# Performance work log

Hardware: AMD Instinct MI355X
Metric: run time of the kernel (lower is better)

## Reference

```python
import jax, jax.numpy as jnp
import numpy as np

B, NN, DEG = 64, 256, 8
N = B * NN
E = N * DEG
IN_N, IN_E = 128, 16
TOOL, PROC = 16, 12
TP = TOOL * PROC
H1 = 384

def _lin(key, i, o, s=0.05):
    k1, k2 = jax.random.split(key)
    return (jax.random.normal(k1, (i, o), jnp.float32) * s,
            jax.random.normal(k2, (o,), jnp.float32) * s)

def setup_inputs():
    ks = jax.random.split(jax.random.key(0), 40)
    inp = {}
    inp["ns"] = jax.random.normal(ks[0], (N, IN_N), jnp.float32)
    inp["es"] = jax.random.normal(ks[1], (E, IN_E), jnp.float32)
    inp["dm"] = jax.random.normal(ks[2], (N, NN), jnp.float32)
    inp["mask_fv"] = (jax.random.uniform(ks[3], (N, TP)) > 0.3).astype(jnp.float32)
    dst = jnp.repeat(jnp.arange(N, dtype=jnp.int32), DEG)  # fixed in-degree DEG
    src = (dst // NN) * NN + jax.random.randint(ks[4], (E,), 0, NN, dtype=jnp.int32)
    inp["src"], inp["dst"] = src, dst
    sizes = [(IN_N, H1), (H1 + 32, H1), (H1, TP)]
    for i, (cin, cout) in enumerate(sizes, 1):
        inp[f"Wm{i}"], inp[f"bm{i}"] = _lin(ks[5 + 3 * i], 2 * cin + IN_E, cin)
        inp[f"Wu{i}"], inp[f"bu{i}"] = _lin(ks[6 + 3 * i], 5 * cin, cout)
        inp[f"bng{i}"] = jnp.ones((cout,), jnp.float32)
        inp[f"bnb{i}"] = jnp.zeros((cout,), jnp.float32)
        inp[f"Wx{i}"], inp[f"bx{i}"] = _lin(ks[7 + 3 * i], cout, cout)
    inp["W1"], inp["b1"] = _lin(ks[20], NN, 64)
    inp["W2"], inp["b2"] = _lin(ks[21], 64, 32)
    inp["W3"], inp["b3"] = _lin(ks[22], NN, 64)
    inp["W4"], inp["b4"] = _lin(ks[23], 64, NN)
    return inp

def pna_conv(src, dst, h, e, Wm, bm, Wu, bu, bng, bnb, Wx, bx, relu_out):
    # DGL PNAConvTower: msg = M(cat(h_src, h_dst, e)); aggregate mean/max/sum/std per dst node;
    # U(cat(h, aggs)); BatchNorm (training stats); mixing Linear + LeakyReLU(0.01).
    cin = h.shape[1]
    msg = h[src] @ Wm[:cin] + h[dst] @ Wm[cin:2 * cin] + e @ Wm[2 * cin:] + bm  # [E, cin]
    cnt = jax.ops.segment_sum(jnp.ones((msg.shape[0],), msg.dtype), dst, N)[:, None]
    s = jax.ops.segment_sum(msg, dst, N)
    mean = s / cnt
    mx = jax.ops.segment_max(msg, dst, N)
    msq = jax.ops.segment_sum(msg * msg, dst, N) / cnt
    std = jnp.sqrt(jax.nn.relu(msq - mean * mean) + 1e-30)
    u = jnp.concatenate([h, mean, mx, s, std], axis=-1) @ Wu + bu  # [N, cout]
    u = (u - u.mean(0)) / jnp.sqrt(u.var(0) + 1e-5) * bng + bnb  # BatchNorm1d, training mode
    out = jax.nn.leaky_relu(u @ Wx + bx, 0.01)  # mixing layer
    return jax.nn.relu(out) if relu_out else out

def reference(ns, es, dm, mask_fv, Wm1, bm1, Wu1, bu1, bng1, bnb1, Wx1, bx1, Wm2, bm2, Wu2, bu2, bng2, bnb2, Wx2, bx2, Wm3, bm3, Wu3, bu3, bng3, bnb3, Wx3, bx3, W1, b1, W2, b2, W3, b3, W4, b4, src, dst):
    d2 = (dm @ W1 + b1) @ W2 + b2  # [N, 32]
    h1 = pna_conv(src, dst, ns, es, Wm1, bm1, Wu1, bu1, bng1, bnb1, Wx1, bx1, True)
    h2 = pna_conv(src, dst, jnp.concatenate([h1, d2], -1), es, Wm2, bm2, Wu2, bu2, bng2, bnb2, Wx2, bx2, True)
    h3 = pna_conv(src, dst, h2, es, Wm3, bm3, Wu3, bu3, bng3, bnb3, Wx3, bx3, False)  # [N, TP]
    nm = h3.max(-1).reshape(B, NN)
    g = jax.nn.sigmoid(jax.nn.relu(nm @ W3 + b3) @ W4 + b4)  # [B, NN]
    feat = (g.reshape(N, 1) * h3).reshape(B, -1)  # [B, NN*TP]
    feat = jnp.where(mask_fv.reshape(B, -1) == 0, -1e5, feat)
    return jax.nn.softmax(feat, -1)
```

## Files before the change

### kernel.cpp

```cpp
#include <hip/hip_runtime.h>
#include <hip/hip_bf16.h>

#define NNODE 16384

typedef short v8s __attribute__((ext_vector_type(8)));
typedef float v4f __attribute__((ext_vector_type(4)));
typedef unsigned short us16;

__device__ __forceinline__ us16 f2bf(float v) {
    unsigned u = __float_as_uint(v);
    unsigned r = (u + 0x7FFF + ((u >> 16) & 1)) >> 16;
    return (us16)r;
}
__device__ __forceinline__ float bf2f(us16 s) {
    return __uint_as_float(((unsigned)s) << 16);
}

template<int EPI, int OUT, int ACC, int BM, int NB>
__global__ __launch_bounds__(256, 3)
void mgemm6(const us16* __restrict__ Ah, const us16* __restrict__ Al,
            int ldA, int K,
            const us16* __restrict__ Bh, const us16* __restrict__ Bl, int KC,
            const float* __restrict__ CfIn, int ldCin,
            float* __restrict__ Cf, us16* __restrict__ Ch, us16* __restrict__ Cl,
            int ldC, int Ncol, const float* __restrict__ bias)
{
    constexpr int MF = BM / 32;
    __shared__ __align__(16) us16 AhS[BM * 64];
    __shared__ __align__(16) us16 AlS[BM * 64];
    const int bm = blockIdx.x * BM;
    const int bn0 = blockIdx.y * (64 * NB);
    const int tid = threadIdx.x;
    const int lane = tid & 63, wid = tid >> 6;
    const int wm = wid >> 1, wn = wid & 1;
    const int r16 = lane & 15, q = lane >> 4;
    v4f acc[NB][MF][2];
#pragma unroll
    for (int b = 0; b < NB; b++)
#pragma unroll
        for (int i = 0; i < MF; i++)
#pragma unroll
            for (int j = 0; j < 2; j++) acc[b][i][j] = (v4f){0.f, 0.f, 0.f, 0.f};

    const int srow = tid >> 3;
    const int sc8  = tid & 7;
    const int cbw  = (bn0 >> 4) + wn * 2;
    const int nK = (K + 63) >> 6;
    for (int s = 0; s < nK; s++) {
        const int k0 = s << 6;
#pragma unroll
        for (int p = 0; p < BM / 32; p++) {
            int row = p * 32 + srow;
            int gk = k0 + sc8 * 8;
            v8s hv = (v8s){0,0,0,0,0,0,0,0};
            v8s lv = (v8s){0,0,0,0,0,0,0,0};
            if (gk < K) {
                size_t go = (size_t)(bm + row) * ldA + gk;
                hv = *(const v8s*)(const void*)(Ah + go);
                lv = *(const v8s*)(const void*)(Al + go);
            }
            int bo = row * 128 + ((sc8 * 16) ^ ((row & 7) << 4));
            *(v8s*)(void*)((char*)AhS + bo) = hv;
            *(v8s*)(void*)((char*)AlS + bo) = lv;
        }
        __syncthreads();
#pragma unroll
        for (int kc = 0; kc < 2; kc++) {
            int kchunk = (k0 >> 5) + kc;
            v8s bfh[NB][2], bfl[NB][2];
#pragma unroll
            for (int nb = 0; nb < NB; nb++)
#pragma unroll
                for (int nf = 0; nf < 2; nf++) {
                    int colblk = cbw + nb * 4 + nf;
                    size_t fo = ((size_t)(colblk * KC + kchunk) * 64 + lane) * 8;
                    bfh[nb][nf] = *(const v8s*)(const void*)(Bh + fo);
                    bfl[nb][nf] = *(const v8s*)(const void*)(Bl + fo);
                }
#pragma unroll
            for (int mf = 0; mf < MF; mf++) {
                int arow = wm * (BM / 2) + mf * 16 + r16;
                int ao = arow * 128 + (((kc * 64) + q * 16) ^ ((arow & 7) << 4));
                v8s ah = *(const v8s*)(const void*)((const char*)AhS + ao);
                v8s al = *(const v8s*)(const void*)((const char*)AlS + ao);
#pragma unroll
                for (int nb = 0; nb < NB; nb++)
#pragma unroll
                    for (int nf = 0; nf < 2; nf++) {
                        acc[nb][mf][nf] = __builtin_amdgcn_mfma_f32_16x16x32_bf16(ah, bfh[nb][nf], acc[nb][mf][nf], 0, 0, 0);
                        acc[nb][mf][nf] = __builtin_amdgcn_mfma_f32_16x16x32_bf16(al, bfh[nb][nf], acc[nb][mf][nf], 0, 0, 0);
                        acc[nb][mf][nf] = __builtin_amdgcn_mfma_f32_16x16x32_bf16(ah, bfl[nb][nf], acc[nb][mf][nf], 0, 0, 0);
                    }
            }
        }
        __syncthreads();
    }
#pragma unroll
    for (int nb = 0; nb < NB; nb++)
#pragma unroll
        for (int mf = 0; mf < MF; mf++)
#pragma unroll
            for (int nf = 0; nf < 2; nf++) {
                int col = bn0 + nb * 64 + wn * 32 + nf * 16 + r16;
                if (col < Ncol) {
                    float bv = bias ? bias[col] : 0.f;
#pragma unroll
                    for (int r = 0; r < 4; r++) {
                        int row = bm + wm * (BM / 2) + mf * 16 + q * 4 + r;
                        float v = acc[nb][mf][nf][r] + bv;
                        if (ACC) v += CfIn[(size_t)row * ldCin + col];
                        if (EPI == 1) v = fmaxf(v, 0.f);
                        if (EPI == 2) v = (v > 0.f) ? v : 0.01f * v;
                        size_t o = (size_t)row * ldC + col;
                        if (OUT == 0) {
                            Cf[o] = v;
                        } else {
                            us16 h = f2bf(v);
                            Ch[o] = h;
                            Cl[o] = f2bf(v - bf2f(h));
                        }
                    }
                }
            }
}

struct FrD {
    const float* W;
    us16* Bh;
    us16* Bl;
    int ldW, Kv, Nv, Na, KC, mode, cin, blk0;
};
struct FrPack { FrD d[16]; int nd; };

__global__ __launch_bounds__(256) void prep_fr_all(FrPack p)
{
    int b = blockIdx.x;
    int i = 0;
    for (int j = 1; j < p.nd; j++) if (b >= p.d[j].blk0) i = j;
    const FrD dd = p.d[i];
    int idx = (b - dd.blk0) * 256 + threadIdx.x;
    if (idx >= dd.Na * dd.KC * 32) return;
    int e = idx & 7, lane = (idx >> 3) & 63, rem = idx >> 9;
    int kchunk = rem % dd.KC, colblk = rem / dd.KC;
    int n = colblk * 16 + (lane & 15);
    int k = kchunk * 32 + (lane >> 4) * 8 + e;
    float v = 0.f;
    if (dd.mode == 0) {
        if (k < dd.Kv && n < dd.Nv) v = dd.W[(size_t)k * dd.ldW + n];
    } else if (dd.mode == 1) {
        int cin = dd.cin, cout = dd.Nv;
        if (n < cout && k < 3 * cin) {
            if (k < cin)          v = dd.W[(size_t)(cin + k) * cout + n] * 0.125f + dd.W[(size_t)(3 * cin + k) * cout + n];
            else if (k < 2 * cin) v = dd.W[(size_t)(2 * cin + (k - cin)) * cout + n];
            else                  v = dd.W[(size_t)(4 * cin + (k - 2 * cin)) * cout + n];
        }
    }
    us16 h = f2bf(v);
    dd.Bh[idx] = h;
    dd.Bl[idx] = f2bf(v - bf2f(h));
}

__global__ void prep_fr_wx(const float* __restrict__ Wx, const float* __restrict__ scale,
                           us16* __restrict__ Bh, us16* __restrict__ Bl,
                           int K, int N, int KC)
{
    int idx = blockIdx.x * 256 + threadIdx.x;
    if (idx >= N * KC * 32) return;
    int e = idx & 7, lane = (idx >> 3) & 63, rem = idx >> 9;
    int kchunk = rem % KC, colblk = rem / KC;
    int n = colblk * 16 + (lane & 15);
    int k = kchunk * 32 + (lane >> 4) * 8 + e;
    float v = (k < K && n < N) ? Wx[(size_t)k * N + n] * scale[k] : 0.f;
    us16 h = f2bf(v);
    Bh[idx] = h;
    Bl[idx] = f2bf(v - bf2f(h));
}

__global__ void w12frag_k(const float* __restrict__ W1, const float* __restrict__ W2,
                          us16* __restrict__ Bh, us16* __restrict__ Bl)
{
    int idx = blockIdx.x * 256 + threadIdx.x;
    if (idx >= 64 * 8 * 32) return;
    int e = idx & 7, lane = (idx >> 3) & 63, rem = idx >> 9;
    int kchunk = rem % 8, colblk = rem / 8;
    int n = colblk * 16 + (lane & 15);
    int k = kchunk * 32 + (lane >> 4) * 8 + e;
    float v = 0.f;
    if (n < 32 && k < 256) {
        for (int j = 0; j < 64; j++) v = fmaf(W1[(size_t)k * 64 + j], W2[(size_t)j * 32 + n], v);
    }
    us16 h = f2bf(v);
    Bh[idx] = h;
    Bl[idx] = f2bf(v - bf2f(h));
}

__global__ void bias12_k(const float* __restrict__ b1, const float* __restrict__ W2,
                         const float* __restrict__ b2, float* __restrict__ b12)
{
    int n = threadIdx.x;
    if (n >= 32) return;
    float s = b2[n];
    for (int j = 0; j < 64; j++) s = fmaf(b1[j], W2[(size_t)j * 32 + n], s);
    b12[n] = s;
}

__global__ __launch_bounds__(256) void bias2p_k(const float* __restrict__ Wx,
    const float* __restrict__ bx, const float* __restrict__ shift,
    float* __restrict__ bias2, int K, int N)
{
    int n = blockIdx.x, tid = threadIdx.x;
    float s = 0.f;
    for (int k = tid; k < K; k += 256) s = fmaf(shift[k], Wx[(size_t)k * N + n], s);
    __shared__ float red[256];
    red[tid] = s; __syncthreads();
    for (int st = 128; st > 0; st >>= 1) { if (tid < st) red[tid] += red[tid + st]; __syncthreads(); }
    if (tid == 0) bias2[n] = red[0] + bx[n];
}

__global__ void prep_biasMU(const float* __restrict__ bm, const float* __restrict__ bu,
                            float* __restrict__ o, int cin, int cout)
{
    int i = blockIdx.x * 256 + threadIdx.x;
    if (i >= 2 * cin + cout) return;
    float v;
    if (i < cin)          v = 0.f;
    else if (i < 2 * cin) v = bm[i - cin];
    else                  v = bu[i - 2 * cin];
    o[i] = v;
}

__global__ void csplit2_k(const float* __restrict__ ns, us16* __restrict__ Xh, us16* __restrict__ Xl,
                          const float* __restrict__ dm, us16* __restrict__ Dh, us16* __restrict__ Dl)
{
    int b = blockIdx.x;
    if (b < 8192) {
        int idx = b * 256 + threadIdx.x;
        int rrow = idx >> 7, c = idx & 127;
        float v = ns[idx];
        us16 h = f2bf(v);
        size_t o = (size_t)rrow * 512 + c;
        Xh[o] = h;
        Xl[o] = f2bf(v - bf2f(h));
    } else {
        int idx = (b - 8192) * 256 + threadIdx.x;
        float v = dm[idx];
        us16 h = f2bf(v);
        Dh[idx] = h;
        Dl[idx] = f2bf(v - bf2f(h));
    }
}

__global__ void csplit_k(const float* __restrict__ src, int ldS, int w,
                         us16* __restrict__ Xh, us16* __restrict__ Xl,
                         int ldX, int offX)
{
    int idx = blockIdx.x * 256 + threadIdx.x;
    if (idx >= NNODE * w) return;
    int rrow = idx / w, c = idx - rrow * w;
    float v = src[(size_t)rrow * ldS + c];
    us16 h = f2bf(v);
    size_t o = (size_t)rrow * ldX + offX + c;
    Xh[o] = h;
    Xl[o] = f2bf(v - bf2f(h));
}

__global__ __launch_bounds__(256)
void agg2_k(const float* __restrict__ H2, const float* __restrict__ es,
            const int* __restrict__ src, const float* __restrict__ Wme,
            us16* __restrict__ Xh, us16* __restrict__ Xl,
            int cin, int ldH, int ldX, int offX)
{
    const int g = blockIdx.x;
    const int c0 = blockIdx.y * 64;
    const int qz = blockIdx.z;
    const int tid = threadIdx.x;
    const int nl = tid >> 6, c = tid & 63;
    const int cc = c0 + c;
    const bool act = cc < cin;
    __shared__ float esl[4][128];
    __shared__ int srcl[512];
    {
        int e0 = g * 2048 + qz * 512;
        for (int i = tid; i < 512; i += 256) srcl[i] = src[e0 + i] - g * 256;
    }
    float wreg[16];
#pragma unroll
    for (int j = 0; j < 16; j++) wreg[j] = act ? Wme[j * cin + cc] : 0.f;
    __syncthreads();
    const float* Hsrc = H2 + (size_t)(g * 256) * ldH + c0;
    const float* Hdst = H2 + (size_t)(g * 256) * ldH + cin + c0;
    for (int i = 0; i < 16; i++) {
        const int vl = qz * 64 + i * 4 + nl;
        {
            const float* ep = es + (size_t)(g * 256 + vl) * 128;
            esl[nl][c] = ep[c];
            esl[nl][64 + c] = ep[64 + c];
        }
        __syncthreads();
        if (act) {
            float hd = Hdst[(size_t)vl * ldH + c];
            float sum = 0.f, sq = 0.f, mx = -INFINITY;
#pragma unroll
            for (int e = 0; e < 8; e++) {
                int sl = srcl[(i * 4 + nl) * 8 + e];
                float m = hd + Hsrc[(size_t)sl * ldH + c];
                float4 e0 = *(const float4*)&esl[nl][e * 16 + 0];
                float4 e1 = *(const float4*)&esl[nl][e * 16 + 4];
                float4 e2 = *(const float4*)&esl[nl][e * 16 + 8];
                float4 e3 = *(const float4*)&esl[nl][e * 16 + 12];
                m = fmaf(e0.x, wreg[0], m);  m = fmaf(e0.y, wreg[1], m);
                m = fmaf(e0.z, wreg[2], m);  m = fmaf(e0.w, wreg[3], m);
                m = fmaf(e1.x, wreg[4], m);  m = fmaf(e1.y, wreg[5], m);
                m = fmaf(e1.z, wreg[6], m);  m = fmaf(e1.w, wreg[7], m);
                m = fmaf(e2.x, wreg[8], m);  m = fmaf(e2.y, wreg[9], m);
                m = fmaf(e2.z, wreg[10], m); m = fmaf(e2.w, wreg[11], m);
                m = fmaf(e3.x, wreg[12], m); m = fmaf(e3.y, wreg[13], m);
                m = fmaf(e3.z, wreg[14], m); m = fmaf(e3.w, wreg[15], m);
                sum += m;
                sq = fmaf(m, m, sq);
                mx = fmaxf(mx, m);
            }
            float mean = sum * 0.125f, msq = sq * 0.125f;
            float stdv = sqrtf(fmaxf(msq - mean * mean, 0.f) + 1e-30f);
            size_t o = (size_t)(g * 256 + vl) * ldX + offX + cc;
            us16 h;
            h = f2bf(sum);  Xh[o] = h;            Xl[o] = f2bf(sum - bf2f(h));
            h = f2bf(mx);   Xh[o + cin] = h;      Xl[o + cin] = f2bf(mx - bf2f(h));
            h = f2bf(stdv); Xh[o + 2 * cin] = h;  Xl[o + 2 * cin] = f2bf(stdv - bf2f(h));
        }
        __syncthreads();
    }
}

__global__ void bnstats1s_k(const us16* __restrict__ uh, const us16* __restrict__ ul,
                            float* __restrict__ part, int cout)
{
    int c = threadIdx.x;
    if (c >= cout) return;
    int r0 = blockIdx.x * 64;
    float s = 0.f, q = 0.f;
    for (int r = r0; r < r0 + 64; r++) {
        size_t o = (size_t)r * cout + c;
        float v = bf2f(uh[o]) + bf2f(ul[o]);
        s += v;
        q = fmaf(v, v, q);
    }
    part[(size_t)blockIdx.x * cout + c] = s;
    part[(size_t)(256 + blockIdx.x) * cout + c] = q;
}

__global__ void bnstats2_k(const float* __restrict__ part, const float* __restrict__ bng,
                           const float* __restrict__ bnb, float* __restrict__ scale,
                           float* __restrict__ shift, int cout)
{
    int c = threadIdx.x;
    if (c >= cout) return;
    float s = 0.f, q = 0.f;
    for (int b = 0; b < 256; b++) { s += part[(size_t)b * cout + c]; q += part[(size_t)(256 + b) * cout + c]; }
    float mean = s / 16384.f;
    float var  = q / 16384.f - mean * mean;
    float sc   = bng[c] / sqrtf(var + 1e-5f);
    scale[c] = sc;
    shift[c] = bnb[c] - mean * sc;
}

__global__ void rowmax_k(const float* __restrict__ h3, float* __restrict__ nm)
{
    int wave = threadIdx.x >> 6;
    int lane = threadIdx.x & 63;
    int node = blockIdx.x * 4 + wave;
    const float* row = h3 + (size_t)node * 192;
    float m = -INFINITY;
    for (int t = lane; t < 192; t += 64) m = fmaxf(m, row[t]);
#pragma unroll
    for (int off = 32; off > 0; off >>= 1) m = fmaxf(m, __shfl_down(m, off, 64));
    if (lane == 0) nm[node] = m;
}

__global__ __launch_bounds__(256) void g_k(const float* __restrict__ nm,
    const float* __restrict__ W3, const float* __restrict__ b3,
    const float* __restrict__ W4, const float* __restrict__ b4,
    float* __restrict__ g)
{
    __shared__ float row[256];
    __shared__ float t1[64];
    int b = blockIdx.x, tid = threadIdx.x;
    row[tid] = nm[b * 256 + tid];
    __syncthreads();
    if (tid < 64) {
        float a = b3[tid];
        for (int k = 0; k < 256; k++) a = fmaf(row[k], W3[k * 64 + tid], a);
        t1[tid] = fmaxf(a, 0.f);
    }
    __syncthreads();
    float a = b4[tid];
    for (int j = 0; j < 64; j++) a = fmaf(t1[j], W4[j * 256 + tid], a);
    g[b * 256 + tid] = 1.f / (1.f + expf(-a));
}

__global__ __launch_bounds__(256) void sm1_k(const float* __restrict__ mask,
    const float* __restrict__ g, const float* __restrict__ h3, float* __restrict__ part)
{
    int b = blockIdx.x, s = blockIdx.y, tid = threadIdx.x;
    float l[24];
#pragma unroll
    for (int t = 0; t < 24; t++) {
        int i = s * 6144 + t * 256 + tid;
        size_t idx = (size_t)b * 49152 + i;
        float mk = mask[idx];
        l[t] = (mk == 0.f) ? -1e5f : g[b * 256 + i / 192] * h3[idx];
    }
    float m = -INFINITY;
#pragma unroll
    for (int t = 0; t < 24; t++) m = fmaxf(m, l[t]);
    __shared__ float red[256];
    red[tid] = m; __syncthreads();
    for (int st = 128; st > 0; st >>= 1) { if (tid < st) red[tid] = fmaxf(red[tid], red[tid + st]); __syncthreads(); }
    m = red[0]; __syncthreads();
    float z = 0.f;
#pragma unroll
    for (int t = 0; t < 24; t++) z += expf(l[t] - m);
    red[tid] = z; __syncthreads();
    for (int st = 128; st > 0; st >>= 1) { if (tid < st) red[tid] += red[tid + st]; __syncthreads(); }
    if (tid == 0) { part[(b * 8 + s) * 2] = m; part[(b * 8 + s) * 2 + 1] = red[0]; }
}

__global__ void sm2_k(const float* __restrict__ part, float* __restrict__ mz)
{
    int b = threadIdx.x;
    if (b >= 64) return;
    float M = -INFINITY;
    for (int s = 0; s < 8; s++) M = fmaxf(M, part[(b * 8 + s) * 2]);
    float Z = 0.f;
    for (int s = 0; s < 8; s++) Z += part[(b * 8 + s) * 2 + 1] * expf(part[(b * 8 + s) * 2] - M);
    mz[b * 2] = M;
    mz[b * 2 + 1] = 1.f / Z;
}

__global__ __launch_bounds__(256) void sm3_k(const float* __restrict__ mask,
    const float* __restrict__ g, const float* __restrict__ h3,
    const float* __restrict__ mz, float* __restrict__ out)
{
    int b = blockIdx.x, s = blockIdx.y, tid = threadIdx.x;
    float M = mz[b * 2], invZ = mz[b * 2 + 1];
#pragma unroll
    for (int t = 0; t < 24; t++) {
        int i = s * 6144 + t * 256 + tid;
        size_t idx = (size_t)b * 49152 + i;
        float mk = mask[idx];
        float v = (mk == 0.f) ? -1e5f : g[b * 256 + i / 192] * h3[idx];
        out[idx] = expf(v - M) * invZ;
    }
}

extern "C" void kernel_launch(void* const* d_in, const int* in_sizes, int n_in,
                              void* d_out, int out_size, void* d_ws, size_t ws_size,
                              hipStream_t stream)
{
    const float* ns   = (const float*)d_in[0];
    const float* es   = (const float*)d_in[1];
    const float* dm   = (const float*)d_in[2];
    const float* mask = (const float*)d_in[3];
    const int*   src  = (const int*)d_in[4];
    const float* Wm1 = (const float*)d_in[6],  *bm1 = (const float*)d_in[7];
    const float* Wu1 = (const float*)d_in[8],  *bu1 = (const float*)d_in[9];
    const float* bng1= (const float*)d_in[10], *bnb1= (const float*)d_in[11];
    const float* Wx1 = (const float*)d_in[12], *bx1 = (const float*)d_in[13];
    const float* Wm2 = (const float*)d_in[14], *bm2 = (const float*)d_in[15];
    const float* Wu2 = (const float*)d_in[16], *bu2 = (const float*)d_in[17];
    const float* bng2= (const float*)d_in[18], *bnb2= (const float*)d_in[19];
    const float* Wx2 = (const float*)d_in[20], *bx2 = (const float*)d_in[21];
    const float* Wm3 = (const float*)d_in[22], *bm3 = (const float*)d_in[23];
    const float* Wu3 = (const float*)d_in[24], *bu3 = (const float*)d_in[25];
    const float* bng3= (const float*)d_in[26], *bnb3= (const float*)d_in[27];
    const float* Wx3 = (const float*)d_in[28], *bx3 = (const float*)d_in[29];
    const float* W1 = (const float*)d_in[30], *b1 = (const float*)d_in[31];
    const float* W2 = (const float*)d_in[32], *b2 = (const float*)d_in[33];
    const float* W3 = (const float*)d_in[34], *b3 = (const float*)d_in[35];
    const float* W4 = (const float*)d_in[36], *b4 = (const float*)d_in[37];
    float* out = (float*)d_out;

    const int N = NNODE;
    char* base = (char*)d_ws;
    size_t off = 0;
    auto alloc = [&](size_t bytes) -> void* {
        void* p = base + off;
        off = (off + bytes + 255) & ~(size_t)255;
        return p;
    };
    us16* Xh = (us16*)alloc((size_t)N * 1728 * 2);
    us16* Xl = (us16*)alloc((size_t)N * 1728 * 2);
    float* H2   = (float*)alloc((size_t)N * 1216 * 4);
    us16* uh = (us16*)alloc((size_t)N * 384 * 2);
    us16* ul = (us16*)alloc((size_t)N * 384 * 2);
    us16* dmh = (us16*)alloc((size_t)N * 256 * 2);
    us16* dml = (us16*)alloc((size_t)N * 256 * 2);
    float* h3b  = (float*)alloc((size_t)N * 192 * 4);
    float* d2f  = (float*)alloc((size_t)N * 32 * 4);
    float* part = (float*)alloc((size_t)512 * 384 * 4);
    float* scale= (float*)alloc(384 * 4);
    float* shift= (float*)alloc(384 * 4);
    float* bias2= (float*)alloc(384 * 4);
    float* b12  = (float*)alloc(32 * 4);
    float* biasMU1 = (float*)alloc(640 * 4);
    float* biasMU2 = (float*)alloc(1216 * 4);
    float* biasMU3 = (float*)alloc(960 * 4);
    float* nm   = (float*)alloc((size_t)N * 4);
    float* gbuf = (float*)alloc((size_t)N * 4);
    float* smp  = (float*)alloc(64 * 8 * 2 * 4);
    float* smz  = (float*)alloc(64 * 2 * 4);
    auto aw = [&](size_t elems) -> us16* { return (us16*)alloc(elems * 2); };
    us16 *BM1h = aw((size_t)640 * 4 * 32),    *BM1l = aw((size_t)640 * 4 * 32);
    us16 *BA1h = aw((size_t)384 * 12 * 32),   *BA1l = aw((size_t)384 * 12 * 32);
    us16 *BX1h = aw((size_t)384 * 12 * 32),   *BX1l = aw((size_t)384 * 12 * 32);
    us16 *BM2h = aw((size_t)1280 * 14 * 32),  *BM2l = aw((size_t)1280 * 14 * 32);
    us16 *BA2h = aw((size_t)384 * 40 * 32),   *BA2l = aw((size_t)384 * 40 * 32);
    us16 *BX2h = aw((size_t)384 * 12 * 32),   *BX2l = aw((size_t)384 * 12 * 32);
    us16 *BM3h = aw((size_t)1024 * 12 * 32),  *BM3l = aw((size_t)1024 * 12 * 32);
    us16 *BA3h = aw((size_t)192 * 36 * 32),   *BA3l = aw((size_t)192 * 36 * 32);
    us16 *BX3h = aw((size_t)192 * 6 * 32),    *BX3l = aw((size_t)192 * 6 * 32);
    us16 *B12h = aw((size_t)64 * 8 * 32),     *B12l = aw((size_t)64 * 8 * 32);

    auto gp = [](size_t n) { return dim3((unsigned)((n + 255) / 256)); };
    auto fsec = [](us16* b, int c0, int KC) { return b + (size_t)(c0 / 16) * KC * 512; };

    FrPack pk;
    int nd = 0, blk = 0;
    auto addD = [&](const float* W, us16* Bh, us16* Bl, int ldW, int Kv, int Nv, int Na, int KC, int mode, int cin) {
        pk.d[nd] = {W, Bh, Bl, ldW, Kv, Nv, Na, KC, mode, cin, blk};
        blk += (Na * KC * 32 + 255) / 256;
        nd++;
    };
    addD(Wm1,             fsec(BM1h,0,4),    fsec(BM1l,0,4),    128, 128, 128, 128, 4, 0, 0);
    addD(Wm1 + 128*128,   fsec(BM1h,128,4),  fsec(BM1l,128,4),  128, 128, 128, 128, 4, 0, 0);
    addD(Wu1,             fsec(BM1h,256,4),  fsec(BM1l,256,4),  384, 128, 384, 384, 4, 0, 0);
    addD(Wu1,             BA1h, BA1l,        0,   0,   384, 384, 12, 1, 128);
    addD(Wm2,             fsec(BM2h,0,14),   fsec(BM2l,0,14),   416, 416, 416, 416, 14, 0, 0);
    addD(Wm2 + 416*416,   fsec(BM2h,416,14), fsec(BM2l,416,14), 416, 416, 416, 416, 14, 0, 0);
    addD(Wu2,             fsec(BM2h,832,14), fsec(BM2l,832,14), 384, 416, 384, 384, 14, 0, 0);
    addD(nullptr,         fsec(BM2h,1216,14),fsec(BM2l,1216,14),0,   0,   0,   64,  14, 2, 0);
    addD(Wu2,             BA2h, BA2l,        0,   0,   384, 384, 40, 1, 416);
    addD(Wm3,             fsec(BM3h,0,12),   fsec(BM3l,0,12),   384, 384, 384, 384, 12, 0, 0);
    addD(Wm3 + 384*384,   fsec(BM3h,384,12), fsec(BM3l,384,12), 384, 384, 384, 384, 12, 0, 0);
    addD(Wu3,             fsec(BM3h,768,12), fsec(BM3l,768,12), 192, 384, 192, 192, 12, 0, 0);
    addD(nullptr,         fsec(BM3h,960,12), fsec(BM3l,960,12), 0,   0,   0,   64,  12, 2, 0);
    addD(Wu3,             BA3h, BA3l,        0,   0,   192, 192, 36, 1, 384);
    pk.nd = nd;

    csplit2_k<<<8192 + 16384, 256, 0, stream>>>(ns, Xh, Xl, dm, dmh, dml);
    prep_fr_all<<<blk, 256, 0, stream>>>(pk);
    w12frag_k<<<gp(64 * 8 * 32), 256, 0, stream>>>(W1, W2, B12h, B12l);
    bias12_k<<<1, 32, 0, stream>>>(b1, W2, b2, b12);
    prep_biasMU<<<gp(640), 256, 0, stream>>>(bm1, bu1, biasMU1, 128, 384);
    prep_biasMU<<<gp(1216), 256, 0, stream>>>(bm2, bu2, biasMU2, 416, 384);
    prep_biasMU<<<gp(960), 256, 0, stream>>>(bm3, bu3, biasMU3, 384, 192);

    mgemm6<0, 0, 0, 128, 1><<<dim3(128, 1), 256, 0, stream>>>(dmh, dml, 256, 256, B12h, B12l, 8,
        nullptr, 0, d2f, nullptr, nullptr, 32, 32, b12);

    mgemm6<0, 0, 0, 128, 2><<<dim3(128, 5), 256, 0, stream>>>(Xh, Xl, 512, 128, BM1h, BM1l, 4,
        nullptr, 0, H2, nullptr, nullptr, 640, 640, biasMU1);
    agg2_k<<<dim3(64, 2, 4), 256, 0, stream>>>(H2, es, src, Wm1 + 2 * 128 * 128, Xh, Xl, 128, 640, 512, 128);
    mgemm6<0, 1, 1, 128, 1><<<dim3(128, 6), 256, 0, stream>>>(Xh + 128, Xl + 128, 512, 384, BA1h, BA1l, 12,
        H2 + 256, 640, nullptr, uh, ul, 384, 384, nullptr);
    bnstats1s_k<<<256, 384, 0, stream>>>(uh, ul, part, 384);
    bnstats2_k<<<1, 384, 0, stream>>>(part, bng1, bnb1, scale, shift, 384);
    prep_fr_wx<<<gp((size_t)384 * 12 * 32), 256, 0, stream>>>(Wx1, scale, BX1h, BX1l, 384, 384, 12);
    bias2p_k<<<384, 256, 0, stream>>>(Wx1, bx1, shift, bias2, 384, 384);
    mgemm6<1, 1, 0, 128, 1><<<dim3(128, 6), 256, 0, stream>>>(uh, ul, 384, 384, BX1h, BX1l, 12,
        nullptr, 0, nullptr, Xh, Xl, 1728, 384, bias2);
    csplit_k<<<gp((size_t)N * 32), 256, 0, stream>>>(d2f, 32, 32, Xh, Xl, 1728, 384);

    mgemm6<0, 0, 0, 128, 2><<<dim3(128, 10), 256, 0, stream>>>(Xh, Xl, 1728, 416, BM2h, BM2l, 14,
        nullptr, 0, H2, nullptr, nullptr, 1216, 1216, biasMU2);
    agg2_k<<<dim3(64, 7, 4), 256, 0, stream>>>(H2, es, src, Wm2 + 2 * 416 * 416, Xh, Xl, 416, 1216, 1728, 416);
    mgemm6<0, 1, 1, 128, 1><<<dim3(128, 6), 256, 0, stream>>>(Xh + 416, Xl + 416, 1728, 1248, BA2h, BA2l, 40,
        H2 + 832, 1216, nullptr, uh, ul, 384, 384, nullptr);
    bnstats1s_k<<<256, 384, 0, stream>>>(uh, ul, part, 384);
    bnstats2_k<<<1, 384, 0, stream>>>(part, bng2, bnb2, scale, shift, 384);
    prep_fr_wx<<<gp((size_t)384 * 12 * 32), 256, 0, stream>>>(Wx2, scale, BX2h, BX2l, 384, 384, 12);
    bias2p_k<<<384, 256, 0, stream>>>(Wx2, bx2, shift, bias2, 384, 384);
    mgemm6<1, 1, 0, 128, 1><<<dim3(128, 6), 256, 0, stream>>>(uh, ul, 384, 384, BX2h, BX2l, 12,
        nullptr, 0, nullptr, Xh, Xl, 1536, 384, bias2);

    mgemm6<0, 0, 0, 128, 2><<<dim3(128, 8), 256, 0, stream>>>(Xh, Xl, 1536, 384, BM3h, BM3l, 12,
        nullptr, 0, H2, nullptr, nullptr, 960, 960, biasMU3);
    agg2_k<<<dim3(64, 6, 4), 256, 0, stream>>>(H2, es, src, Wm3 + 2 * 384 * 384, Xh, Xl, 384, 960, 1536, 384);
    mgemm6<0, 1, 1, 64, 1><<<dim3(256, 3), 256, 0, stream>>>(Xh + 384, Xl + 384, 1536, 1152, BA3h, BA3l, 36,
        H2 + 768, 960, nullptr, uh, ul, 192, 192, nullptr);
    bnstats1s_k<<<256, 384, 0, stream>>>(uh, ul, part, 192);
    bnstats2_k<<<1, 384, 0, stream>>>(part, bng3, bnb3, scale, shift, 192);
    prep_fr_wx<<<gp((size_t)192 * 6 * 32), 256, 0, stream>>>(Wx3, scale, BX3h, BX3l, 192, 192, 6);
    bias2p_k<<<192, 256, 0, stream>>>(Wx3, bx3, shift, bias2, 192, 192);
    mgemm6<2, 0, 0, 64, 1><<<dim3(256, 3), 256, 0, stream>>>(uh, ul, 192, 192, BX3h, BX3l, 6,
        nullptr, 0, h3b, nullptr, nullptr, 192, 192, bias2);

    rowmax_k<<<N / 4, 256, 0, stream>>>(h3b, nm);
    g_k<<<64, 256, 0, stream>>>(nm, W3, b3, W4, b4, gbuf);
    sm1_k<<<dim3(64, 8), 256, 0, stream>>>(mask, gbuf, h3b, smp);
    sm2_k<<<1, 64, 0, stream>>>(smp, smz);
    sm3_k<<<dim3(64, 8), 256, 0, stream>>>(mask, gbuf, h3b, smz, out);
}
```

Measured before the change: 691.2 us.

## Prefetch next A tile into registers and switch GEMMs to 64-row tiles

Replaces the GEMM kernel with a variant that fixes the row tile at 64 and register-prefetches the next K-slice of A while MFMAs run on the current shared-memory tile. B fragments for both k-chunks are loaded up front. Launch grids are reshaped to match, with NB=2 on several GEMMs so each block covers 128 columns instead of 64. The aim is to hide global-load latency and rebalance the grid across CUs, at the cost of more registers per thread and possibly lower occupancy.

Result: faster. 671.2 us (-2.9%).

```diff
diff --git a/kernel.cpp b/kernel.cpp
--- a/kernel.cpp
+++ b/kernel.cpp
@@ -16,29 +16,28 @@
     return __uint_as_float(((unsigned)s) << 16);
 }
 
-template<int EPI, int OUT, int ACC, int BM, int NB>
+template<int EPI, int OUT, int ACC, int NB>
 __global__ __launch_bounds__(256, 3)
-void mgemm6(const us16* __restrict__ Ah, const us16* __restrict__ Al,
+void mgemm7(const us16* __restrict__ Ah, const us16* __restrict__ Al,
             int ldA, int K,
             const us16* __restrict__ Bh, const us16* __restrict__ Bl, int KC,
             const float* __restrict__ CfIn, int ldCin,
             float* __restrict__ Cf, us16* __restrict__ Ch, us16* __restrict__ Cl,
             int ldC, int Ncol, const float* __restrict__ bias)
 {
-    constexpr int MF = BM / 32;
-    __shared__ __align__(16) us16 AhS[BM * 64];
-    __shared__ __align__(16) us16 AlS[BM * 64];
-    const int bm = blockIdx.x * BM;
+    __shared__ __align__(16) us16 AhS[64 * 64];
+    __shared__ __align__(16) us16 AlS[64 * 64];
+    const int bm = blockIdx.x * 64;
     const int bn0 = blockIdx.y * (64 * NB);
     const int tid = threadIdx.x;
     const int lane = tid & 63, wid = tid >> 6;
     const int wm = wid >> 1, wn = wid & 1;
     const int r16 = lane & 15, q = lane >> 4;
-    v4f acc[NB][MF][2];
+    v4f acc[NB][2][2];
 #pragma unroll
     for (int b = 0; b < NB; b++)
 #pragma unroll
-        for (int i = 0; i < MF; i++)
+        for (int i = 0; i < 2; i++)
 #pragma unroll
             for (int j = 0; j < 2; j++) acc[b][i][j] = (v4f){0.f, 0.f, 0.f, 0.f};
 
@@ -46,40 +45,69 @@
     const int sc8  = tid & 7;
     const int cbw  = (bn0 >> 4) + wn * 2;
     const int nK = (K + 63) >> 6;
+
+    v8s ph[2], pl[2];
+    {
+        int gk = sc8 * 8;
+#pragma unroll
+        for (int p = 0; p < 2; p++) {
+            int row = p * 32 + srow;
+            ph[p] = (v8s){0,0,0,0,0,0,0,0};
+            pl[p] = (v8s){0,0,0,0,0,0,0,0};
+            if (gk < K) {
+                size_t go = (size_t)(bm + row) * ldA + gk;
+                ph[p] = *(const v8s*)(const void*)(Ah + go);
+                pl[p] = *(const v8s*)(const void*)(Al + go);
+            }
+        }
+    }
+
     for (int s = 0; s < nK; s++) {
         const int k0 = s << 6;
-#pragma unroll
-        for (int p = 0; p < BM / 32; p++) {
+        __syncthreads();
+#pragma unroll
+        for (int p = 0; p < 2; p++) {
             int row = p * 32 + srow;
-            int gk = k0 + sc8 * 8;
-            v8s hv = (v8s){0,0,0,0,0,0,0,0};
-            v8s lv = (v8s){0,0,0,0,0,0,0,0};
-            if (gk < K) {
-                size_t go = (size_t)(bm + row) * ldA + gk;
-                hv = *(const v8s*)(const void*)(Ah + go);
-                lv = *(const v8s*)(const void*)(Al + go);
-            }
             int bo = row * 128 + ((sc8 * 16) ^ ((row & 7) << 4));
-            *(v8s*)(void*)((char*)AhS + bo) = hv;
-            *(v8s*)(void*)((char*)AlS + bo) = lv;
+            *(v8s*)(void*)((char*)AhS + bo) = ph[p];
+            *(v8s*)(void*)((char*)AlS + bo) = pl[p];
         }
         __syncthreads();
+        v8s bfh[2][NB][2], bfl[2][NB][2];
 #pragma unroll
         for (int kc = 0; kc < 2; kc++) {
             int kchunk = (k0 >> 5) + kc;
-            v8s bfh[NB][2], bfl[NB][2];
 #pragma unroll
             for (int nb = 0; nb < NB; nb++)
 #pragma unroll
                 for (int nf = 0; nf < 2; nf++) {
                     int colblk = cbw + nb * 4 + nf;
                     size_t fo = ((size_t)(colblk * KC + kchunk) * 64 + lane) * 8;
-                    bfh[nb][nf] = *(const v8s*)(const void*)(Bh + fo);
-                    bfl[nb][nf] = *(const v8s*)(const void*)(Bl + fo);
+                    bfh[kc][nb][nf] = *(const v8s*)(const void*)(Bh + fo);
+                    bfl[kc][nb][nf] = *(const v8s*)(const void*)(Bl + fo);
                 }
-#pragma unroll
-            for (int mf = 0; mf < MF; mf++) {
-                int arow = wm * (BM / 2) + mf * 16 + r16;
+        }
+        if (s + 1 < nK) {
+            int gk = (k0 + 64) + sc8 * 8;
+#pragma unroll
+            for (int p = 0; p < 2; p++) {
+                int row = p * 32 + srow;
+                v8s hv = (v8s){0,0,0,0,0,0,0,0};
+                v8s lv = (v8s){0,0,0,0,0,0,0,0};
+                if (gk < K) {
+                    size_t go = (size_t)(bm + row) * ldA + gk;
+                    hv = *(const v8s*)(const void*)(Ah + go);
+                    lv = *(const v8s*)(const void*)(Al + go);
+                }
+                ph[p] = hv;
+                pl[p] = lv;
+            }
+        }
+#pragma unroll
+        for (int kc = 0; kc < 2; kc++) {
+#pragma unroll
+            for (int mf = 0; mf < 2; mf++) {
+                int arow = wm * 32 + mf * 16 + r16;
                 int ao = arow * 128 + (((kc * 64) + q * 16) ^ ((arow & 7) << 4));
                 v8s ah = *(const v8s*)(const void*)((const char*)AhS + ao);
                 v8s al = *(const v8s*)(const void*)((const char*)AlS + ao);
@@ -87,18 +115,17 @@
                 for (int nb = 0; nb < NB; nb++)
 #pragma unroll
                     for (int nf = 0; nf < 2; nf++) {
-                        acc[nb][mf][nf] = __builtin_amdgcn_mfma_f32_16x16x32_bf16(ah, bfh[nb][nf], acc[nb][mf][nf], 0, 0, 0);
-                        acc[nb][mf][nf] = __builtin_amdgcn_mfma_f32_16x16x32_bf16(al, bfh[nb][nf], acc[nb][mf][nf], 0, 0, 0);
-                        acc[nb][mf][nf] = __builtin_amdgcn_mfma_f32_16x16x32_bf16(ah, bfl[nb][nf], acc[nb][mf][nf], 0, 0, 0);
+                        acc[nb][mf][nf] = __builtin_amdgcn_mfma_f32_16x16x32_bf16(ah, bfh[kc][nb][nf], acc[nb][mf][nf], 0, 0, 0);
+                        acc[nb][mf][nf] = __builtin_amdgcn_mfma_f32_16x16x32_bf16(al, bfh[kc][nb][nf], acc[nb][mf][nf], 0, 0, 0);
+                        acc[nb][mf][nf] = __builtin_amdgcn_mfma_f32_16x16x32_bf16(ah, bfl[kc][nb][nf], acc[nb][mf][nf], 0, 0, 0);
                     }
             }
         }
-        __syncthreads();
     }
 #pragma unroll
     for (int nb = 0; nb < NB; nb++)
 #pragma unroll
-        for (int mf = 0; mf < MF; mf++)
+        for (int mf = 0; mf < 2; mf++)
 #pragma unroll
             for (int nf = 0; nf < 2; nf++) {
                 int col = bn0 + nb * 64 + wn * 32 + nf * 16 + r16;
@@ -106,7 +133,7 @@
                     float bv = bias ? bias[col] : 0.f;
 #pragma unroll
                     for (int r = 0; r < 4; r++) {
-                        int row = bm + wm * (BM / 2) + mf * 16 + q * 4 + r;
+                        int row = bm + wm * 32 + mf * 16 + q * 4 + r;
                         float v = acc[nb][mf][nf][r] + bv;
                         if (ACC) v += CfIn[(size_t)row * ldCin + col];
                         if (EPI == 1) v = fmaxf(v, 0.f);
@@ -555,44 +582,44 @@
     prep_biasMU<<<gp(1216), 256, 0, stream>>>(bm2, bu2, biasMU2, 416, 384);
     prep_biasMU<<<gp(960), 256, 0, stream>>>(bm3, bu3, biasMU3, 384, 192);
 
-    mgemm6<0, 0, 0, 128, 1><<<dim3(128, 1), 256, 0, stream>>>(dmh, dml, 256, 256, B12h, B12l, 8,
+    mgemm7<0, 0, 0, 1><<<dim3(256, 1), 256, 0, stream>>>(dmh, dml, 256, 256, B12h, B12l, 8,
         nullptr, 0, d2f, nullptr, nullptr, 32, 32, b12);
 
-    mgemm6<0, 0, 0, 128, 2><<<dim3(128, 5), 256, 0, stream>>>(Xh, Xl, 512, 128, BM1h, BM1l, 4,
+    mgemm7<0, 0, 0, 2><<<dim3(256, 5), 256, 0, stream>>>(Xh, Xl, 512, 128, BM1h, BM1l, 4,
         nullptr, 0, H2, nullptr, nullptr, 640, 640, biasMU1);
     agg2_k<<<dim3(64, 2, 4), 256, 0, stream>>>(H2, es, src, Wm1 + 2 * 128 * 128, Xh, Xl, 128, 640, 512, 128);
-    mgemm6<0, 1, 1, 128, 1><<<dim3(128, 6), 256, 0, stream>>>(Xh + 128, Xl + 128, 512, 384, BA1h, BA1l, 12,
+    mgemm7<0, 1, 1, 2><<<dim3(256, 3), 256, 0, stream>>>(Xh + 128, Xl + 128, 512, 384, BA1h, BA1l, 12,
         H2 + 256, 640, nullptr, uh, ul, 384, 384, nullptr);
     bnstats1s_k<<<256, 384, 0, stream>>>(uh, ul, part, 384);
     bnstats2_k<<<1, 384, 0, stream>>>(part, bng1, bnb1, scale, shift, 384);
     prep_fr_wx<<<gp((size_t)384 * 12 * 32), 256, 0, stream>>>(Wx1, scale, BX1h, BX1l, 384, 384, 12);
     bias2p_k<<<384, 256, 0, stream>>>(Wx1, bx1, shift, bias2, 384, 384);
-    mgemm6<1, 1, 0, 128, 1><<<dim3(128, 6), 256, 0, stream>>>(uh, ul, 384, 384, BX1h, BX1l, 12,
+    mgemm7<1, 1, 0, 2><<<dim3(256, 3), 256, 0, stream>>>(uh, ul, 384, 384, BX1h, BX1l, 12,
         nullptr, 0, nullptr, Xh, Xl, 1728, 384, bias2);
     csplit_k<<<gp((size_t)N * 32), 256, 0, stream>>>(d2f, 32, 32, Xh, Xl, 1728, 384);
 
-    mgemm6<0, 0, 0, 128, 2><<<dim3(128, 10), 256, 0, stream>>>(Xh, Xl, 1728, 416, BM2h, BM2l, 14,
+    mgemm7<0, 0, 0, 2><<<dim3(256, 10), 256, 0, stream>>>(Xh, Xl, 1728, 416, BM2h, BM2l, 14,
         nullptr, 0, H2, nullptr, nullptr, 1216, 1216, biasMU2);
     agg2_k<<<dim3(64, 7, 4), 256, 0, stream>>>(H2, es, src, Wm2 + 2 * 416 * 416, Xh, Xl, 416, 1216, 1728, 416);
-    mgemm6<0, 1, 1, 128, 1><<<dim3(128, 6), 256, 0, stream>>>(Xh + 416, Xl + 416, 1728, 1248, BA2h, BA2l, 40,
+    mgemm7<0, 1, 1, 2><<<dim3(256, 3), 256, 0, stream>>>(Xh + 416, Xl + 416, 1728, 1248, BA2h, BA2l, 40,
         H2 + 832, 1216, nullptr, uh, ul, 384, 384, nullptr);
     bnstats1s_k<<<256, 384, 0, stream>>>(uh, ul, part, 384);
     bnstats2_k<<<1, 384, 0, stream>>>(part, bng2, bnb2, scale, shift, 384);
     prep_fr_wx<<<gp((size_t)384 * 12 * 32), 256, 0, stream>>>(Wx2, scale, BX2h, BX2l, 384, 384, 12);
     bias2p_k<<<384, 256, 0, stream>>>(Wx2, bx2, shift, bias2, 384, 384);
-    mgemm6<1, 1, 0, 128, 1><<<dim3(128, 6), 256, 0, stream>>>(uh, ul, 384, 384, BX2h, BX2l, 12,
+    mgemm7<1, 1, 0, 2><<<dim3(256, 3), 256, 0, stream>>>(uh, ul, 384, 384, BX2h, BX2l, 12,
         nullptr, 0, nullptr, Xh, Xl, 1536, 384, bias2);
 
-    mgemm6<0, 0, 0, 128, 2><<<dim3(128, 8), 256, 0, stream>>>(Xh, Xl, 1536, 384, BM3h, BM3l, 12,
+    mgemm7<0, 0, 0, 2><<<dim3(256, 8), 256, 0, stream>>>(Xh, Xl, 1536, 384, BM3h, BM3l, 12,
         nullptr, 0, H2, nullptr, nullptr, 960, 960, biasMU3);
     agg2_k<<<dim3(64, 6, 4), 256, 0, stream>>>(H2, es, src, Wm3 + 2 * 384 * 384, Xh, Xl, 384, 960, 1536, 384);
-    mgemm6<0, 1, 1, 64, 1><<<dim3(256, 3), 256, 0, stream>>>(Xh + 384, Xl + 384, 1536, 1152, BA3h, BA3l, 36,
+    mgemm7<0, 1, 1, 1><<<dim3(256, 3), 256, 0, stream>>>(Xh + 384, Xl + 384, 1536, 1152, BA3h, BA3l, 36,
         H2 + 768, 960, nullptr, uh, ul, 192, 192, nullptr);
     bnstats1s_k<<<256, 384, 0, stream>>>(uh, ul, part, 192);
     bnstats2_k<<<1, 384, 0, stream>>>(part, bng3, bnb3, scale, shift, 192);
     prep_fr_wx<<<gp((size_t)192 * 6 * 32), 256, 0, stream>>>(Wx3, scale, BX3h, BX3l, 192, 192, 6);
     bias2p_k<<<192, 256, 0, stream>>>(Wx3, bx3, shift, bias2, 192, 192);
-    mgemm6<2, 0, 0, 64, 1><<<dim3(256, 3), 256, 0, stream>>>(uh, ul, 192, 192, BX3h, BX3l, 6,
+    mgemm7<2, 0, 0, 1><<<dim3(256, 3), 256, 0, stream>>>(uh, ul, 192, 192, BX3h, BX3l, 6,
         nullptr, 0, h3b, nullptr, nullptr, 192, 192, bias2);
 
     rowmax_k<<<N / 4, 256, 0, stream>>>(h3b, nm);
```
